# Kernel optimization log

Hardware: AMD Instinct MI355X
Metric: run time of the kernel (lower is better)

The kernel has to match this reference:

```python
import jax, jax.numpy as jnp
import numpy as np

EMPTY_IDX = 6  # relabeling of the original -1 ('EMPTY') expert to row 6 of the stacked tables


def setup_inputs() -> dict:
    key = jax.random.key(0)
    k1, k2, k3, k4, k5, k6 = jax.random.split(key, 6)
    B, L, H, T, E = 32, 2048, 768, 12, 7
    return {
        "sequence_output": jax.random.normal(k1, (B, L, H), dtype=jnp.float32),
        "module_net_w": jax.random.normal(k2, (E, H, H), dtype=jnp.float32),
        "span_net_w": jax.random.normal(k3, (E, H, 2), dtype=jnp.float32),
        "turns": jax.random.randint(k4, (B, T, 2), 0, L),
        "key_phrase_span": jax.random.randint(k5, (B, T, 2), 0, L),
        "module_index": jax.random.randint(k6, (B, T), 0, E),
    }


def reference(sequence_output, module_net_w, span_net_w, turns, key_phrase_span, module_index):
    seq = sequence_output            # [B, L, H]
    B, L, H = seq.shape
    T = turns.shape[1]
    f32 = seq.dtype

    eidx = module_index              # [B, T], 0..6 (6 == EMPTY, original -1)
    mod_mask = (eidx != EMPTY_IDX).astype(f32)            # module_index != -1
    start_pos = turns[:, :, 0]       # [B, T] turn start token positions
    turns_mask = (start_pos >= 0).astype(f32)             # turns[:,:,0] != -1

    # context_hidden_step = sequence_output[arange(B), start] for every step
    ctx = jnp.take_along_axis(seq, start_pos[:, :, None], axis=1)   # [B, T, H]

    # einsum('bh,bhz,blz->blz'): (ctx @ W_expert) broadcast-multiplied with seq.
    # Compute ctx @ W for ALL experts (tables are tiny), then gather per (b, t).
    cW_all = jnp.einsum('bth,ehz->btez', ctx, module_net_w)         # [B, T, 7, H]
    gidx = jnp.broadcast_to(eidx[:, :, None, None], (B, T, 1, H))
    cW = jnp.take_along_axis(cW_all, gidx, axis=2).squeeze(2)       # [B, T, H]

    span_w = span_net_w[eidx]        # [B, T, H, 2] per-sample expert span weights
    # logits[b,t,l,k] = sum_z seq[b,l,z] * cW[b,t,z] * span_w[b,t,z,k]
    v = cW[..., None] * span_w                                      # [B, T, H, 2]
    logits = jnp.einsum('blz,btzk->btlk', seq, v)                   # [B, T, L, 2]

    # CrossEntropyLoss(ignore_index=-1, reduction='none') over the L axis
    logsm = jax.nn.log_softmax(logits, axis=2)                      # [B, T, L, 2]
    tgt = key_phrase_span[:, :, :T][:, :T]  # [B, T, 2]
    tgt = key_phrase_span
    safe = jnp.clip(tgt, 0, L - 1)                                  # [B, T, 2]
    picked = jnp.take_along_axis(logsm, safe[:, :, None, :], axis=2).squeeze(2)  # [B, T, 2]
    ce = jnp.where(tgt >= 0, -picked, jnp.zeros((), f32))           # [B, T, 2]
    step_loss = 0.5 * (ce[..., 0] + ce[..., 1]) * mod_mask          # [B, T]

    loss = (step_loss * turns_mask).sum() / turns_mask.sum()
    return loss
```

## Files before the change

### kernel.cpp

```cpp
#include <hip/hip_runtime.h>
#include <math.h>

#define Bz 32
#define Lz 2048
#define Hz 768
#define Tz 12
#define Ez 7
#define EMPTYIDX 6
#define NCOL 24
#define NITEM (Bz * Tz)
#define LCHUNK 128
#define NCHUNK 16

__global__ void k0_compact(const int* __restrict__ midx,
                           int* __restrict__ off, int* __restrict__ items) {
    __shared__ int cnt[Ez];
    __shared__ int offs[Ez + 1];
    int tid = threadIdx.x;
    if (tid < Ez) cnt[tid] = 0;
    __syncthreads();
    int e = midx[tid];
    e = min(max(e, 0), Ez - 1);
    int r = atomicAdd(&cnt[e], 1);
    __syncthreads();
    if (tid == 0) {
        int acc = 0;
        for (int j = 0; j < Ez; ++j) { offs[j] = acc; acc += cnt[j]; }
        offs[Ez] = acc;
    }
    __syncthreads();
    items[offs[e] + r] = tid;
    if (tid <= Ez) off[tid] = offs[tid];
}

#define K1A_ZC 3
#define K1A_HB 48
#define K1A_HC 16
__global__ void k1a_cw(const float* __restrict__ seq, const float* __restrict__ W,
                       const int* __restrict__ turns,
                       const int* __restrict__ off, const int* __restrict__ items,
                       float* __restrict__ pc) {
    int bx = blockIdx.x;
    int e  = bx % Ez;
    int zc = (bx / Ez) % K1A_ZC;
    int hc = bx / (Ez * K1A_ZC);
    int z  = zc * 256 + threadIdx.x;
    int h0 = hc * K1A_HB;
    int off0 = off[e];
    int cnt  = off[e + 1] - off0;
    const float* Wb = W + ((size_t)e * Hz + h0) * Hz + z;
    float w[K1A_HB];
#pragma unroll
    for (int j = 0; j < K1A_HB; ++j) w[j] = Wb[(size_t)j * Hz];

    for (int n = 0; n < cnt; ++n) {
        int i  = items[off0 + n];
        int b  = i / Tz;
        int st = turns[2 * i];
        st = min(max(st, 0), Lz - 1);
        const float* c = seq + ((size_t)(b * Lz + st)) * Hz + h0;
        float acc = 0.f;
#pragma unroll
        for (int j = 0; j < K1A_HB; ++j) acc = fmaf(c[j], w[j], acc);
        pc[((size_t)hc * NITEM + i) * Hz + z] = acc;
    }
}

__global__ void k1b_v(const float* __restrict__ pc, const float* __restrict__ spanw,
                      const int* __restrict__ midx, float* __restrict__ v) {
    int idx = blockIdx.x * 256 + threadIdx.x;
    int i = idx / Hz;
    int z = idx - i * Hz;
    float cw = 0.f;
#pragma unroll
    for (int hc = 0; hc < K1A_HC; ++hc)
        cw += pc[((size_t)hc * NITEM + i) * Hz + z];
    int e = midx[i];
    e = min(max(e, 0), Ez - 1);
    int b = i / Tz, t = i - b * Tz;
    size_t vb = ((size_t)(b * NCOL + t * 2)) * Hz + z;
    v[vb]      = cw * spanw[(e * Hz + z) * 2 + 0];
    v[vb + Hz] = cw * spanw[(e * Hz + z) * 2 + 1];
}

#define BKP 64
#define NPH (Hz / BKP)

typedef float4 F4;

__device__ __forceinline__ float dot32(const float* __restrict__ vp,
    F4 a0, F4 a1, F4 a2, F4 a3, F4 a4, F4 a5, F4 a6, F4 a7) {
    const F4* vq = (const F4*)vp;
    F4 q0 = vq[0], q1 = vq[1], q2 = vq[2], q3 = vq[3],
       q4 = vq[4], q5 = vq[5], q6 = vq[6], q7 = vq[7];
    float s0 = 0.f, s1 = 0.f, s2 = 0.f, s3 = 0.f;
    s0 = fmaf(a0.x, q0.x, s0); s1 = fmaf(a0.y, q0.y, s1);
    s2 = fmaf(a0.z, q0.z, s2); s3 = fmaf(a0.w, q0.w, s3);
    s0 = fmaf(a1.x, q1.x, s0); s1 = fmaf(a1.y, q1.y, s1);
    s2 = fmaf(a1.z, q1.z, s2); s3 = fmaf(a1.w, q1.w, s3);
    s0 = fmaf(a2.x, q2.x, s0); s1 = fmaf(a2.y, q2.y, s1);
    s2 = fmaf(a2.z, q2.z, s2); s3 = fmaf(a2.w, q2.w, s3);
    s0 = fmaf(a3.x, q3.x, s0); s1 = fmaf(a3.y, q3.y, s1);
    s2 = fmaf(a3.z, q3.z, s2); s3 = fmaf(a3.w, q3.w, s3);
    s0 = fmaf(a4.x, q4.x, s0); s1 = fmaf(a4.y, q4.y, s1);
    s2 = fmaf(a4.z, q4.z, s2); s3 = fmaf(a4.w, q4.w, s3);
    s0 = fmaf(a5.x, q5.x, s0); s1 = fmaf(a5.y, q5.y, s1);
    s2 = fmaf(a5.z, q5.z, s2); s3 = fmaf(a5.w, q5.w, s3);
    s0 = fmaf(a6.x, q6.x, s0); s1 = fmaf(a6.y, q6.y, s1);
    s2 = fmaf(a6.z, q6.z, s2); s3 = fmaf(a6.w, q6.w, s3);
    s0 = fmaf(a7.x, q7.x, s0); s1 = fmaf(a7.y, q7.y, s1);
    s2 = fmaf(a7.z, q7.z, s2); s3 = fmaf(a7.w, q7.w, s3);
    return (s0 + s1) + (s2 + s3);
}

#define C_LIST(X) X(0) X(1) X(2) X(3) X(4) X(5) X(6) X(7) X(8) X(9) X(10) X(11) \
                  X(12) X(13) X(14) X(15) X(16) X(17) X(18) X(19) X(20) X(21) X(22) X(23)

__global__ __launch_bounds__(256, 2)
void k2_logits(const float* __restrict__ seq, const float* __restrict__ v,
               const int* __restrict__ kps,
               float* __restrict__ pm, float* __restrict__ ps,
               float* __restrict__ picked) {
    int bx  = blockIdx.x;
    int b   = bx / NCHUNK;
    int ch  = bx % NCHUNK;
    int l0  = ch * LCHUNK;
    int tid = threadIdx.x;
    int r   = tid & (LCHUNK - 1);
    int kh  = __builtin_amdgcn_readfirstlane(tid >> 7);

    __shared__ float at[LCHUNK][BKP];
    __shared__ float lg[LCHUNK][NCOL + 1];
    __shared__ float redm[NCOL][4], reds[NCOL][4];
    __shared__ int   ksafe[NCOL];

    if (tid < NCOL) {
        int t0 = kps[b * NCOL + tid];
        ksafe[tid] = min(max(t0, 0), Lz - 1);
    }

#define DECL_ACC(n) float c##n = 0.f;
    C_LIST(DECL_ACC)
#undef DECL_ACC

    const float* A = seq + ((size_t)b * Lz + l0) * Hz;
    const float* V = v + (size_t)b * NCOL * Hz;

    int rb   = tid >> 4;
    int cq   = tid & 15;
    int slot = ((cq ^ (rb & 15)) << 2);
    const float* Ab0 = A + (size_t)rb * Hz + (cq << 2);
    float* Sb = &at[0][0] + rb * BKP + slot;

    int rx = r & 15;
    const float* arow = &at[r][0];
    const float* ap0 = arow + (((kh * 8 + 0) ^ rx) << 2);
    const float* ap1 = arow + (((kh * 8 + 1) ^ rx) << 2);
    const float* ap2 = arow + (((kh * 8 + 2) ^ rx) << 2);
    const float* ap3 = arow + (((kh * 8 + 3) ^ rx) << 2);
    const float* ap4 = arow + (((kh * 8 + 4) ^ rx) << 2);
    const float* ap5 = arow + (((kh * 8 + 5) ^ rx) << 2);
    const float* ap6 = arow + (((kh * 8 + 6) ^ rx) << 2);
    const float* ap7 = arow + (((kh * 8 + 7) ^ rx) << 2);

    F4 g0, g1, g2, g3, g4, g5, g6, g7;
#define LOADG(KOFF) do { const float* Ap_ = Ab0 + (KOFF);            \
        g0 = *(const F4*)&Ap_[0 * 16 * Hz];                          \
        g1 = *(const F4*)&Ap_[1 * 16 * Hz];                          \
        g2 = *(const F4*)&Ap_[2 * 16 * Hz];                          \
        g3 = *(const F4*)&Ap_[3 * 16 * Hz];                          \
        g4 = *(const F4*)&Ap_[4 * 16 * Hz];                          \
        g5 = *(const F4*)&Ap_[5 * 16 * Hz];                          \
        g6 = *(const F4*)&Ap_[6 * 16 * Hz];                          \
        g7 = *(const F4*)&Ap_[7 * 16 * Hz]; } while (0)

    LOADG(0);

#pragma unroll 1
    for (int ph = 0; ph < NPH; ++ph) {
        __syncthreads();
        *(F4*)&Sb[0 * 1024] = g0;  *(F4*)&Sb[1 * 1024] = g1;
        *(F4*)&Sb[2 * 1024] = g2;  *(F4*)&Sb[3 * 1024] = g3;
        *(F4*)&Sb[4 * 1024] = g4;  *(F4*)&Sb[5 * 1024] = g5;
        *(F4*)&Sb[6 * 1024] = g6;  *(F4*)&Sb[7 * 1024] = g7;
        __syncthreads();
        if (ph + 1 < NPH) LOADG((ph + 1) * BKP);

        F4 a0 = *(const F4*)ap0, a1 = *(const F4*)ap1,
           a2 = *(const F4*)ap2, a3 = *(const F4*)ap3,
           a4 = *(const F4*)ap4, a5 = *(const F4*)ap5,
           a6 = *(const F4*)ap6, a7 = *(const F4*)ap7;

        const float* Vp = V + ph * BKP + kh * 32;
#define DO_COL(n) c##n += dot32(Vp + (n) * Hz, a0, a1, a2, a3, a4, a5, a6, a7);
        C_LIST(DO_COL)
#undef DO_COL
    }
#undef LOADG

    __syncthreads();
    if (kh == 1) {
#define ST_LG(n) lg[r][n] = c##n;
        C_LIST(ST_LG)
#undef ST_LG
    }
    __syncthreads();
    if (kh == 0) {
        int grow = l0 + r;
#define MG_LG(n) { c##n += lg[r][n]; lg[r][n] = c##n;                 \
                   if (ksafe[n] == grow) picked[b * NCOL + (n)] = c##n; }
        C_LIST(MG_LG)
#undef MG_LG
    }
    __syncthreads();

    if (tid < 96) {
        int c = tid >> 2, rg = tid & 3;
        float m = lg[rg * 32][c];
        for (int rr = rg * 32 + 1; rr < rg * 32 + 32; ++rr)
            m = fmaxf(m, lg[rr][c]);
        float s = 0.f;
        for (int rr = rg * 32; rr < rg * 32 + 32; ++rr)
            s += expf(lg[rr][c] - m);
        redm[c][rg] = m; reds[c][rg] = s;
    }
    __syncthreads();
    if (tid < NCOL) {
        float m = redm[tid][0];
        for (int j = 1; j < 4; ++j) m = fmaxf(m, redm[tid][j]);
        float s = 0.f;
        for (int j = 0; j < 4; ++j) s += reds[tid][j] * expf(redm[tid][j] - m);
        pm[((size_t)b * NCOL + tid) * NCHUNK + ch] = m;
        ps[((size_t)b * NCOL + tid) * NCHUNK + ch] = s;
    }
}

__global__ void k4_final(const int* __restrict__ midx, const int* __restrict__ turns,
                         const int* __restrict__ kps,
                         const float* __restrict__ pm, const float* __restrict__ ps,
                         const float* __restrict__ picked, float* __restrict__ out) {
    int tid = threadIdx.x;
    int i = tid;
    int b = i / Tz, t = i % Tz;
    int e = midx[i];
    float modm  = (e != EMPTYIDX) ? 1.f : 0.f;
    float tmask = (turns[2 * i] >= 0) ? 1.f : 0.f;
    float ce[2];
#pragma unroll
    for (int k = 0; k < 2; ++k) {
        int c = t * 2 + k;
        const float* pmr = pm + ((size_t)b * NCOL + c) * NCHUNK;
        const float* psr = ps + ((size_t)b * NCOL + c) * NCHUNK;
        float m = pmr[0];
        for (int chn = 1; chn < NCHUNK; ++chn) m = fmaxf(m, pmr[chn]);
        float s = 0.f;
        for (int chn = 0; chn < NCHUNK; ++chn) s += psr[chn] * expf(pmr[chn] - m);
        float lse = m + logf(s);
        int tgt = kps[2 * i + k];
        ce[k] = (tgt >= 0) ? (lse - picked[b * NCOL + c]) : 0.f;
    }
    float contrib = 0.5f * (ce[0] + ce[1]) * modm * tmask;

    __shared__ float wsum[6], wmask[6];
    float sl = contrib, sm = tmask;
    for (int o = 32; o > 0; o >>= 1) {
        sl += __shfl_down(sl, o, 64);
        sm += __shfl_down(sm, o, 64);
    }
    int w = tid >> 6, lane = tid & 63;
    if (lane == 0) { wsum[w] = sl; wmask[w] = sm; }
    __syncthreads();
    if (tid == 0) {
        float a = 0.f, mk = 0.f;
        for (int ww = 0; ww < 6; ++ww) { a += wsum[ww]; mk += wmask[ww]; }
        out[0] = a / mk;
    }
}

extern "C" void kernel_launch(void* const* d_in, const int* in_sizes, int n_in,
                              void* d_out, int out_size, void* d_ws, size_t ws_size,
                              hipStream_t stream) {
    const float* seq   = (const float*)d_in[0];
    const float* W     = (const float*)d_in[1];
    const float* spanw = (const float*)d_in[2];
    const int*   turns = (const int*)d_in[3];
    const int*   kps   = (const int*)d_in[4];
    const int*   midx  = (const int*)d_in[5];
    float* out = (float*)d_out;

    char* ws = (char*)d_ws;
    int*   off    = (int*)(ws + 0);
    int*   items  = (int*)(ws + 256);
    float* pc     = (float*)(ws + 2048);
    float* v      = (float*)(ws + 2048 + 18874368);
    float* pm     = (float*)(ws + 2048 + 18874368 + 2359296);
    float* ps     = (float*)(ws + 2048 + 18874368 + 2359296 + 49152);
    float* picked = (float*)(ws + 2048 + 18874368 + 2359296 + 98304);

    hipLaunchKernelGGL(k0_compact, dim3(1), dim3(NITEM), 0, stream, midx, off, items);
    hipLaunchKernelGGL(k1a_cw, dim3(Ez * K1A_ZC * K1A_HC), dim3(256), 0, stream,
                       seq, W, turns, off, items, pc);
    hipLaunchKernelGGL(k1b_v, dim3((NITEM * Hz) / 256), dim3(256), 0, stream,
                       pc, spanw, midx, v);
    hipLaunchKernelGGL(k2_logits, dim3(Bz * NCHUNK), dim3(256), 0, stream,
                       seq, v, kps, pm, ps, picked);
    hipLaunchKernelGGL(k4_final, dim3(1), dim3(NITEM), 0, stream,
                       midx, turns, kps, pm, ps, picked, out);
}
```

Before: 409.7 us.

## Halve L-chunk per block and split K across four wave groups

The logits kernel now processes 64 sequence rows per block instead of 128, doubling the grid, and splits each 64-wide K phase into four 16-wide slices, one per 64-thread group. Partial sums are merged through three shared buffers. Per-thread registers drop, so the launch bound is raised to 4 blocks per CU for better occupancy and latency hiding. The cost is that each block re-reads the v vectors for half as many rows, doubling v traffic, and the partial-sum merge has more steps. The workspace offsets are enlarged to fit the doubled chunk count.

```diff
diff --git a/kernel.cpp b/kernel.cpp
--- a/kernel.cpp
+++ b/kernel.cpp
@@ -9,8 +9,8 @@
 #define EMPTYIDX 6
 #define NCOL 24
 #define NITEM (Bz * Tz)
-#define LCHUNK 128
-#define NCHUNK 16
+#define LCHUNK 64
+#define NCHUNK 32
 
 __global__ void k0_compact(const int* __restrict__ midx,
                            int* __restrict__ off, int* __restrict__ items) {
@@ -88,11 +88,10 @@
 
 typedef float4 F4;
 
-__device__ __forceinline__ float dot32(const float* __restrict__ vp,
-    F4 a0, F4 a1, F4 a2, F4 a3, F4 a4, F4 a5, F4 a6, F4 a7) {
+__device__ __forceinline__ float dot16(const float* __restrict__ vp,
+                                       F4 a0, F4 a1, F4 a2, F4 a3) {
     const F4* vq = (const F4*)vp;
-    F4 q0 = vq[0], q1 = vq[1], q2 = vq[2], q3 = vq[3],
-       q4 = vq[4], q5 = vq[5], q6 = vq[6], q7 = vq[7];
+    F4 q0 = vq[0], q1 = vq[1], q2 = vq[2], q3 = vq[3];
     float s0 = 0.f, s1 = 0.f, s2 = 0.f, s3 = 0.f;
     s0 = fmaf(a0.x, q0.x, s0); s1 = fmaf(a0.y, q0.y, s1);
     s2 = fmaf(a0.z, q0.z, s2); s3 = fmaf(a0.w, q0.w, s3);
@@ -102,21 +101,13 @@
     s2 = fmaf(a2.z, q2.z, s2); s3 = fmaf(a2.w, q2.w, s3);
     s0 = fmaf(a3.x, q3.x, s0); s1 = fmaf(a3.y, q3.y, s1);
     s2 = fmaf(a3.z, q3.z, s2); s3 = fmaf(a3.w, q3.w, s3);
-    s0 = fmaf(a4.x, q4.x, s0); s1 = fmaf(a4.y, q4.y, s1);
-    s2 = fmaf(a4.z, q4.z, s2); s3 = fmaf(a4.w, q4.w, s3);
-    s0 = fmaf(a5.x, q5.x, s0); s1 = fmaf(a5.y, q5.y, s1);
-    s2 = fmaf(a5.z, q5.z, s2); s3 = fmaf(a5.w, q5.w, s3);
-    s0 = fmaf(a6.x, q6.x, s0); s1 = fmaf(a6.y, q6.y, s1);
-    s2 = fmaf(a6.z, q6.z, s2); s3 = fmaf(a6.w, q6.w, s3);
-    s0 = fmaf(a7.x, q7.x, s0); s1 = fmaf(a7.y, q7.y, s1);
-    s2 = fmaf(a7.z, q7.z, s2); s3 = fmaf(a7.w, q7.w, s3);
     return (s0 + s1) + (s2 + s3);
 }
 
 #define C_LIST(X) X(0) X(1) X(2) X(3) X(4) X(5) X(6) X(7) X(8) X(9) X(10) X(11) \
                   X(12) X(13) X(14) X(15) X(16) X(17) X(18) X(19) X(20) X(21) X(22) X(23)
 
-__global__ __launch_bounds__(256, 2)
+__global__ __launch_bounds__(256, 4)
 void k2_logits(const float* __restrict__ seq, const float* __restrict__ v,
                const int* __restrict__ kps,
                float* __restrict__ pm, float* __restrict__ ps,
@@ -127,10 +118,12 @@
     int l0  = ch * LCHUNK;
     int tid = threadIdx.x;
     int r   = tid & (LCHUNK - 1);
-    int kh  = __builtin_amdgcn_readfirstlane(tid >> 7);
+    int kq  = __builtin_amdgcn_readfirstlane(tid >> 6);
 
     __shared__ float at[LCHUNK][BKP];
-    __shared__ float lg[LCHUNK][NCOL + 1];
+    __shared__ float bufA[LCHUNK][NCOL + 1];
+    __shared__ float bufB[LCHUNK][NCOL + 1];
+    __shared__ float bufC[LCHUNK][NCOL + 1];
     __shared__ float redm[NCOL][4], reds[NCOL][4];
     __shared__ int   ksafe[NCOL];
 
@@ -148,31 +141,23 @@
 
     int rb   = tid >> 4;
     int cq   = tid & 15;
-    int slot = ((cq ^ (rb & 15)) << 2);
+    int slot = ((cq ^ rb) << 2);
     const float* Ab0 = A + (size_t)rb * Hz + (cq << 2);
     float* Sb = &at[0][0] + rb * BKP + slot;
 
     int rx = r & 15;
     const float* arow = &at[r][0];
-    const float* ap0 = arow + (((kh * 8 + 0) ^ rx) << 2);
-    const float* ap1 = arow + (((kh * 8 + 1) ^ rx) << 2);
-    const float* ap2 = arow + (((kh * 8 + 2) ^ rx) << 2);
-    const float* ap3 = arow + (((kh * 8 + 3) ^ rx) << 2);
-    const float* ap4 = arow + (((kh * 8 + 4) ^ rx) << 2);
-    const float* ap5 = arow + (((kh * 8 + 5) ^ rx) << 2);
-    const float* ap6 = arow + (((kh * 8 + 6) ^ rx) << 2);
-    const float* ap7 = arow + (((kh * 8 + 7) ^ rx) << 2);
-
-    F4 g0, g1, g2, g3, g4, g5, g6, g7;
+    const float* ap0 = arow + (((kq * 4 + 0) ^ rx) << 2);
+    const float* ap1 = arow + (((kq * 4 + 1) ^ rx) << 2);
+    const float* ap2 = arow + (((kq * 4 + 2) ^ rx) << 2);
+    const float* ap3 = arow + (((kq * 4 + 3) ^ rx) << 2);
+
+    F4 g0, g1, g2, g3;
 #define LOADG(KOFF) do { const float* Ap_ = Ab0 + (KOFF);            \
         g0 = *(const F4*)&Ap_[0 * 16 * Hz];                          \
         g1 = *(const F4*)&Ap_[1 * 16 * Hz];                          \
         g2 = *(const F4*)&Ap_[2 * 16 * Hz];                          \
-        g3 = *(const F4*)&Ap_[3 * 16 * Hz];                          \
-        g4 = *(const F4*)&Ap_[4 * 16 * Hz];                          \
-        g5 = *(const F4*)&Ap_[5 * 16 * Hz];                          \
-        g6 = *(const F4*)&Ap_[6 * 16 * Hz];                          \
-        g7 = *(const F4*)&Ap_[7 * 16 * Hz]; } while (0)
+        g3 = *(const F4*)&Ap_[3 * 16 * Hz]; } while (0)
 
     LOADG(0);
 
@@ -181,47 +166,51 @@
         __syncthreads();
         *(F4*)&Sb[0 * 1024] = g0;  *(F4*)&Sb[1 * 1024] = g1;
         *(F4*)&Sb[2 * 1024] = g2;  *(F4*)&Sb[3 * 1024] = g3;
-        *(F4*)&Sb[4 * 1024] = g4;  *(F4*)&Sb[5 * 1024] = g5;
-        *(F4*)&Sb[6 * 1024] = g6;  *(F4*)&Sb[7 * 1024] = g7;
         __syncthreads();
         if (ph + 1 < NPH) LOADG((ph + 1) * BKP);
 
         F4 a0 = *(const F4*)ap0, a1 = *(const F4*)ap1,
-           a2 = *(const F4*)ap2, a3 = *(const F4*)ap3,
-           a4 = *(const F4*)ap4, a5 = *(const F4*)ap5,
-           a6 = *(const F4*)ap6, a7 = *(const F4*)ap7;
-
-        const float* Vp = V + ph * BKP + kh * 32;
-#define DO_COL(n) c##n += dot32(Vp + (n) * Hz, a0, a1, a2, a3, a4, a5, a6, a7);
+           a2 = *(const F4*)ap2, a3 = *(const F4*)ap3;
+
+        const float* Vp = V + ph * BKP + kq * 16;
+#define DO_COL(n) c##n += dot16(Vp + (n) * Hz, a0, a1, a2, a3);
         C_LIST(DO_COL)
 #undef DO_COL
     }
 #undef LOADG
 
     __syncthreads();
-    if (kh == 1) {
-#define ST_LG(n) lg[r][n] = c##n;
-        C_LIST(ST_LG)
-#undef ST_LG
-    }
-    __syncthreads();
-    if (kh == 0) {
+    if (kq == 1) {
+#define ST_A(n) bufA[r][n] = c##n;
+        C_LIST(ST_A)
+#undef ST_A
+    } else if (kq == 2) {
+#define ST_B(n) bufB[r][n] = c##n;
+        C_LIST(ST_B)
+#undef ST_B
+    } else if (kq == 3) {
+#define ST_C(n) bufC[r][n] = c##n;
+        C_LIST(ST_C)
+#undef ST_C
+    }
+    __syncthreads();
+    if (kq == 0) {
         int grow = l0 + r;
-#define MG_LG(n) { c##n += lg[r][n]; lg[r][n] = c##n;                 \
-                   if (ksafe[n] == grow) picked[b * NCOL + (n)] = c##n; }
-        C_LIST(MG_LG)
-#undef MG_LG
+#define MG(n) { c##n += bufA[r][n] + bufB[r][n] + bufC[r][n]; bufA[r][n] = c##n; \
+                if (ksafe[n] == grow) picked[b * NCOL + (n)] = c##n; }
+        C_LIST(MG)
+#undef MG
     }
     __syncthreads();
 
     if (tid < 96) {
         int c = tid >> 2, rg = tid & 3;
-        float m = lg[rg * 32][c];
-        for (int rr = rg * 32 + 1; rr < rg * 32 + 32; ++rr)
-            m = fmaxf(m, lg[rr][c]);
+        float m = bufA[rg * 16][c];
+        for (int rr = rg * 16 + 1; rr < rg * 16 + 16; ++rr)
+            m = fmaxf(m, bufA[rr][c]);
         float s = 0.f;
-        for (int rr = rg * 32; rr < rg * 32 + 32; ++rr)
-            s += expf(lg[rr][c] - m);
+        for (int rr = rg * 16; rr < rg * 16 + 16; ++rr)
+            s += expf(bufA[rr][c] - m);
         redm[c][rg] = m; reds[c][rg] = s;
     }
     __syncthreads();
@@ -294,8 +283,8 @@
     float* pc     = (float*)(ws + 2048);
     float* v      = (float*)(ws + 2048 + 18874368);
     float* pm     = (float*)(ws + 2048 + 18874368 + 2359296);
-    float* ps     = (float*)(ws + 2048 + 18874368 + 2359296 + 49152);
-    float* picked = (float*)(ws + 2048 + 18874368 + 2359296 + 98304);
+    float* ps     = (float*)(ws + 2048 + 18874368 + 2359296 + 98304);
+    float* picked = (float*)(ws + 2048 + 18874368 + 2359296 + 196608);
 
     hipLaunchKernelGGL(k0_compact, dim3(1), dim3(NITEM), 0, stream, midx, off, items);
     hipLaunchKernelGGL(k1a_cw, dim3(Ez * K1A_ZC * K1A_HC), dim3(256), 0, stream,
```

Result: faster. 379.5 us (-7.4%).
